# Kernel optimization log

Measured on AMD Instinct MI355X. Metric: run time of the kernel, lower is better.

## Reference

```python
import jax, jax.numpy as jnp
import numpy as np

N = 4096
C = 64
B = 4
DIST_THRESHOLD = 0.5
ALPHA = 0.01
NEG_INF = -1e15


def setup_inputs() -> dict:
    key = jax.random.key(0)
    k1, k2, k3, k4, k5 = jax.random.split(key, 5)
    x = jax.random.normal(k1, (B, N, C), dtype=jnp.float32)
    dist_mat = jax.random.uniform(k2, (N, N), dtype=jnp.float32)
    proj_w = jax.random.normal(k3, (N, C, C), dtype=jnp.float32) / np.sqrt(C)
    proj_b = jax.random.normal(k4, (N, C), dtype=jnp.float32) * 0.01
    a_w = jax.random.normal(k5, (N, 2 * C), dtype=jnp.float32) / np.sqrt(2 * C)
    return {"x": x, "dist_mat": dist_mat, "proj_w": proj_w, "proj_b": proj_b, "a_w": a_w}


def reference(x, dist_mat, proj_w, proj_b, a_w):
    # Adjacency: (0 < dist < threshold), diagonal forced to 1.
    adj = (dist_mat > 0) & (dist_mat < DIST_THRESHOLD)
    adj = adj | jnp.eye(N, dtype=bool)

    # Per-node projection (GraphDense): h[b,n,:] = x[b,n,:] @ proj_w[n] + proj_b[n]
    h = jnp.einsum('bnc,nco->bno', x, proj_w) + proj_b  # [B, N, C]

    # Attention score: a[j] . concat(h_i, h_j) without materializing [B,N,N,2C].
    a_src, a_dst = a_w[:, :C], a_w[:, C:]               # each [N, C]
    s = jnp.einsum('bic,jc->bij', h, a_src) + jnp.einsum('bjc,jc->bj', h, a_dst)[:, None, :]
    s = jnp.where(s >= 0, s, ALPHA * s)                 # LeakyReLU
    s = jnp.where(adj[None, :, :], s, NEG_INF)          # mask non-edges
    att = jax.nn.softmax(s, axis=-1)                    # [B, N, N]

    # Weighted aggregation over neighbors.
    y = jnp.einsum('bij,bjc->bic', att, h)              # [B, N, C]
    return y
```

## Files before the change

kernel.cpp:

```cpp
#include <hip/hip_runtime.h>

#define N 4096
#define C 64
#define B 4
#define SHIFT 12.0f

typedef __attribute__((ext_vector_type(8))) short short8;
typedef __attribute__((ext_vector_type(4))) short s16x4;
typedef __attribute__((ext_vector_type(4))) float f32x4;
typedef unsigned long long u64;

#define MFMA16(a, b, c) __builtin_amdgcn_mfma_f32_16x16x32_bf16(a, b, c, 0, 0, 0)

__device__ __forceinline__ short f2bf(float f) {
    unsigned u = __builtin_bit_cast(unsigned, f);
    u += 0x7fffu + ((u >> 16) & 1u);
    return (short)(u >> 16);
}

__global__ __launch_bounds__(256) void mask_kernel(const float* __restrict__ dist,
                                                   u64* __restrict__ msk) {
    const int wave = threadIdx.x >> 6, lane = threadIdx.x & 63;
    const int i = blockIdx.x * 4 + wave;
    const float* row = dist + (size_t)i * N;
#pragma unroll 8
    for (int jb = 0; jb < N / 64; jb++) {
        float d = row[jb * 64 + lane];
        u64 m = __ballot(d > 0.f && d < 0.5f);
        int dj = i - jb * 64;
        if (dj >= 0 && dj < 64) m |= (1ull << dj);
        if (lane == 0) msk[(size_t)i * (N / 64) + jb] = m;
    }
}

__global__ __launch_bounds__(256) void proj_kernel(
    const float* __restrict__ x,
    const float* __restrict__ proj_w,
    const float* __restrict__ proj_b,
    const float* __restrict__ a_w,
    short* __restrict__ h_bf,
    short* __restrict__ a_srcb,
    float* __restrict__ e2)
{
    __shared__ float lds_x[4][B][C];

    const int tid = threadIdx.x;
    const int wave = tid >> 6;
    const int lane = tid & 63;
    const int g = lane >> 4;
    const int o4 = lane & 15;
    const int n = blockIdx.x * 4 + wave;
    const float* Wn = proj_w + (size_t)n * C * C;

#pragma unroll
    for (int b = 0; b < B; b++)
        lds_x[wave][b][lane] = x[((size_t)b * N + n) * C + lane];

    float4 wbuf[16];
#pragma unroll
    for (int p = 0; p < 16; p++)
        wbuf[p] = *(const float4*)(Wn + (p * 4 + g) * C + o4 * 4);

    float acc[B][4];
#pragma unroll
    for (int b = 0; b < B; b++)
#pragma unroll
        for (int r = 0; r < 4; r++) acc[b][r] = 0.f;

#pragma unroll
    for (int p = 0; p < 16; p++) {
        float xs[B];
#pragma unroll
        for (int b = 0; b < B; b++) xs[b] = lds_x[wave][b][p * 4 + g];
#pragma unroll
        for (int b = 0; b < B; b++) {
            acc[b][0] = fmaf(xs[b], wbuf[p].x, acc[b][0]);
            acc[b][1] = fmaf(xs[b], wbuf[p].y, acc[b][1]);
            acc[b][2] = fmaf(xs[b], wbuf[p].z, acc[b][2]);
            acc[b][3] = fmaf(xs[b], wbuf[p].w, acc[b][3]);
        }
    }

#pragma unroll
    for (int b = 0; b < B; b++)
#pragma unroll
        for (int r = 0; r < 4; r++) {
            acc[b][r] += __shfl_xor(acc[b][r], 16, 64);
            acc[b][r] += __shfl_xor(acc[b][r], 32, 64);
        }

    float4 pb4 = *(const float4*)(proj_b + (size_t)n * C + o4 * 4);
#pragma unroll
    for (int b = 0; b < B; b++) {
        acc[b][0] += pb4.x; acc[b][1] += pb4.y;
        acc[b][2] += pb4.z; acc[b][3] += pb4.w;
    }

    float hg[4];
#pragma unroll
    for (int r = 0; r < 4; r++) {
        float v01 = (g & 1) ? acc[1][r] : acc[0][r];
        float v23 = (g & 1) ? acc[3][r] : acc[2][r];
        hg[r] = (g & 2) ? v23 : v01;
    }

    {
        s16x4 hv;
#pragma unroll
        for (int r = 0; r < 4; r++) hv[r] = f2bf(hg[r]);
        *(s16x4*)&h_bf[((size_t)g * N + n) * C + o4 * 4] = hv;
    }

    if (g == 0) {
        float4 as4 = *(const float4*)(a_w + (size_t)n * 2 * C + o4 * 4);
        s16x4 av;
        av[0] = f2bf(as4.x); av[1] = f2bf(as4.y);
        av[2] = f2bf(as4.z); av[3] = f2bf(as4.w);
        *(s16x4*)&a_srcb[(size_t)n * C + o4 * 4] = av;
    }

    {
        float4 ad4 = *(const float4*)(a_w + (size_t)n * 2 * C + C + o4 * 4);
        float s = hg[0] * ad4.x + hg[1] * ad4.y + hg[2] * ad4.z + hg[3] * ad4.w;
        s += __shfl_xor(s, 1, 64);
        s += __shfl_xor(s, 2, 64);
        s += __shfl_xor(s, 4, 64);
        s += __shfl_xor(s, 8, 64);
        if (o4 == 0) e2[g * N + n] = s - SHIFT;
    }
}

__global__ __launch_bounds__(256) void transpose_kernel(const short* __restrict__ h_bf,
                                                        short* __restrict__ hT_bf) {
    __shared__ short tile[64][72];
    const int t = threadIdx.x;
    const int b = blockIdx.y;
    const int n0 = blockIdx.x * 64;
    {
        int r = t >> 2, cs = (t & 3) * 16;
        const short* src = h_bf + ((size_t)b * N + n0 + r) * C + cs;
#pragma unroll
        for (int q = 0; q < 4; q++)
            *(s16x4*)&tile[r][cs + q * 4] = *(const s16x4*)(src + q * 4);
    }
    __syncthreads();
    {
        int c = t >> 2, ns = (t & 3) * 16;
        short v[16];
#pragma unroll
        for (int k = 0; k < 16; k++) v[k] = tile[ns + k][c];
        short* dst = hT_bf + (size_t)b * C * N + (size_t)c * N + n0 + ns;
        *(short8*)dst = *(short8*)&v[0];
        *(short8*)(dst + 8) = *(short8*)&v[8];
    }
}

__global__ __launch_bounds__(256) void attn_kernel(
    const u64* __restrict__ msk,
    const short* __restrict__ h_bf,
    const short* __restrict__ hT_bf,
    const short* __restrict__ a_srcb,
    const float* __restrict__ e2,
    float* __restrict__ part_y,
    float* __restrict__ part_l,
    int JS, int S, int mode)
{
    __shared__ float lds_e2[4][512];

    const int tid = threadIdx.x;
    const int wave = tid >> 6;
    const int lane = tid & 63;
    const int cl = lane & 15;
    const int rg = lane >> 4;
    const int rg8 = rg * 8;
    const int b = wave;
    const int sy = blockIdx.x % S;
    const int ix = blockIdx.x / S;
    const int i0 = ix * 32;
    const int jbeg = sy * JS;
    const bool e2lds = (JS <= 512);

    if (e2lds) {
        for (int q = lane * 4; q < JS; q += 256)
            *(f32x4*)&lds_e2[wave][q] = *(const f32x4*)(e2 + (size_t)b * N + jbeg + q);
    }

    short8 bfr[2][2];
#pragma unroll
    for (int u = 0; u < 2; u++) {
        const short* hrow = h_bf + ((size_t)b * N + i0 + u * 16 + cl) * C;
        bfr[u][0] = *(const short8*)(hrow + rg8);
        bfr[u][1] = *(const short8*)(hrow + 32 + rg8);
    }

    const u64* mr[2] = {msk + (size_t)(i0 + cl) * (N / 64),
                        msk + (size_t)(i0 + 16 + cl) * (N / 64)};

    f32x4 yacc[2][4];
#pragma unroll
    for (int u = 0; u < 2; u++)
#pragma unroll
        for (int t = 0; t < 4; t++) { f32x4 z = {0.f, 0.f, 0.f, 0.f}; yacc[u][t] = z; }
    float l_s[2] = {0.f, 0.f};

    const int jr = ((cl >> 2) << 3) | (cl & 3);
    const short* abase = a_srcb + (size_t)(jr) * C + rg8;

    short8 an0[4], an1[4];
#pragma unroll
    for (int t = 0; t < 4; t++) {
        const short* arow = abase + (size_t)(jbeg + (t >> 1) * 32 + (t & 1) * 4) * C;
        an0[t] = *(const short8*)(arow);
        an1[t] = *(const short8*)(arow + 32);
    }
    u64 mb0 = mr[0][jbeg >> 6], mb1 = mr[1][jbeg >> 6];

    for (int j0 = jbeg; j0 < jbeg + JS; j0 += 64) {
        const int jp = (j0 + 64 < jbeg + JS) ? j0 + 64 : jbeg;
        const u64 mb[2] = {mb0, mb1};

        short8 a0[4], a1[4];
#pragma unroll
        for (int t = 0; t < 4; t++) { a0[t] = an0[t]; a1[t] = an1[t]; }

        short8 h0[4], h1[4];
#pragma unroll
        for (int t = 0; t < 4; t++) {
            const short* hc = hT_bf + (size_t)b * C * N + (size_t)(t * 16 + cl) * N + j0 + rg8;
            h0[t] = *(const short8*)(hc);
            h1[t] = *(const short8*)(hc + 32);
        }
#pragma unroll
        for (int t = 0; t < 4; t++) {
            const short* arow = abase + (size_t)(jp + (t >> 1) * 32 + (t & 1) * 4) * C;
            an0[t] = *(const short8*)(arow);
            an1[t] = *(const short8*)(arow + 32);
        }
        u64 nb0 = mr[0][jp >> 6], nb1 = mr[1][jp >> 6];

        f32x4 st[2][4];
#pragma unroll
        for (int t = 0; t < 4; t++) {
            const int tq = t >> 1, tr = t & 1;
            const int off = tq * 32 + tr * 4 + rg8;
            f32x4 eq;
            if (e2lds) eq = *(const f32x4*)&lds_e2[wave][j0 - jbeg + off];
            else       eq = *(const f32x4*)(e2 + (size_t)b * N + j0 + off);
            const int sh = rg8 + tr * 4;
#pragma unroll
            for (int u = 0; u < 2; u++) {
                unsigned w32 = tq ? (unsigned)(mb[u] >> 32) : (unsigned)mb[u];
                unsigned ws = w32 >> sh;
                f32x4 z;
#pragma unroll
                for (int r = 0; r < 4; r++)
                    z[r] = ((ws >> r) & 1u) ? eq[r] : -1e30f;
                z = MFMA16(a0[t], bfr[u][0], z);
                z = MFMA16(a1[t], bfr[u][1], z);
                st[u][t] = z;
            }
        }

        short8 pa[2][2];
#pragma unroll
        for (int u = 0; u < 2; u++) {
            float ls = 0.f;
            short8 q0, q1;
#pragma unroll
            for (int t = 0; t < 4; t++) {
#pragma unroll
                for (int r = 0; r < 4; r++) {
                    float sv = st[u][t][r];
                    float pv = __expf(fmaxf(sv, fmaf(0.01f, sv, -11.88f)));
                    ls += pv;
                    short bv = f2bf(pv);
                    if (t < 2) q0[(t & 1) * 4 + r] = bv;
                    else       q1[(t & 1) * 4 + r] = bv;
                }
            }
            l_s[u] += ls;
            pa[u][0] = q0;
            pa[u][1] = q1;
        }

#pragma unroll
        for (int t = 0; t < 4; t++) {
            yacc[0][t] = MFMA16(pa[0][0], h0[t], yacc[0][t]);
            yacc[0][t] = MFMA16(pa[0][1], h1[t], yacc[0][t]);
            yacc[1][t] = MFMA16(pa[1][0], h0[t], yacc[1][t]);
            yacc[1][t] = MFMA16(pa[1][1], h1[t], yacc[1][t]);
        }
        mb0 = nb0; mb1 = nb1;
    }

#pragma unroll
    for (int u = 0; u < 2; u++) {
        l_s[u] += __shfl_xor(l_s[u], 16, 64);
        l_s[u] += __shfl_xor(l_s[u], 32, 64);
    }

    if (mode) {
#pragma unroll
        for (int u = 0; u < 2; u++) {
            int li = __builtin_bit_cast(int, l_s[u]);
            f32x4 l4;
#pragma unroll
            for (int r = 0; r < 4; r++)
                l4[r] = __builtin_bit_cast(float,
                        __builtin_amdgcn_ds_bpermute((rg * 4 + r) << 2, li));
#pragma unroll
            for (int t = 0; t < 4; t++)
#pragma unroll
                for (int r = 0; r < 4; r++)
                    part_y[((size_t)b * N + i0 + u * 16 + rg * 4 + r) * C + t * 16 + cl] =
                        yacc[u][t][r] / l4[r];
        }
    } else {
        size_t sb = (size_t)(sy * B + b) * N;
#pragma unroll
        for (int u = 0; u < 2; u++) {
#pragma unroll
            for (int t = 0; t < 4; t++)
#pragma unroll
                for (int r = 0; r < 4; r++)
                    part_y[(sb + i0 + u * 16 + rg * 4 + r) * C + t * 16 + cl] = yacc[u][t][r];
            if (lane < 16) part_l[sb + i0 + u * 16 + lane] = l_s[u];
        }
    }
}

__global__ __launch_bounds__(256) void combine_kernel(
    const float* __restrict__ part_y, const float* __restrict__ part_l,
    float* __restrict__ out, int S)
{
    int g = blockIdx.x * 256 + threadIdx.x;
    int c4 = (g & 15) * 4;
    int row = (g >> 4) & (N - 1);
    int b = g >> 16;
    int bn = b * N + row;
    f32x4 y = {0.f, 0.f, 0.f, 0.f};
    float l = 0.f;
    if (S == 8) {
#pragma unroll
        for (int s = 0; s < 8; s++) {
            l += part_l[s * (B * N) + bn];
            f32x4 v = *(const f32x4*)&part_y[((size_t)s * B * N + bn) * C + c4];
#pragma unroll
            for (int r = 0; r < 4; r++) y[r] += v[r];
        }
    } else {
        for (int s = 0; s < S; s++) {
            l += part_l[s * (B * N) + bn];
            f32x4 v = *(const f32x4*)&part_y[((size_t)s * B * N + bn) * C + c4];
#pragma unroll
            for (int r = 0; r < 4; r++) y[r] += v[r];
        }
    }
    float inv = 1.f / l;
    f32x4 o;
#pragma unroll
    for (int r = 0; r < 4; r++) o[r] = y[r] * inv;
    *(f32x4*)&out[(size_t)g * 4] = o;
}

extern "C" void kernel_launch(void* const* d_in, const int* in_sizes, int n_in,
                              void* d_out, int out_size, void* d_ws, size_t ws_size,
                              hipStream_t stream) {
    const float* x      = (const float*)d_in[0];
    const float* dist   = (const float*)d_in[1];
    const float* proj_w = (const float*)d_in[2];
    const float* proj_b = (const float*)d_in[3];
    const float* a_w    = (const float*)d_in[4];
    float* out = (float*)d_out;

    char* ws = (char*)d_ws;
    short* h_bf   = (short*)(ws);
    short* hT_bf  = (short*)(ws + (2u << 20));
    short* a_srcb = (short*)(ws + (4u << 20));
    float* e2     = (float*)(ws + (4u << 20) + (512u << 10));
    u64*   msk    = (u64*)  (ws + (5u << 20));
    float* part_l = (float*)(ws + (7u << 20));
    float* part_y = (float*)(ws + (8u << 20));

    proj_kernel<<<N / 4, 256, 0, stream>>>(x, proj_w, proj_b, a_w, h_bf, a_srcb, e2);
    transpose_kernel<<<dim3(N / 64, B), 256, 0, stream>>>(h_bf, hT_bf);
    mask_kernel<<<N / 4, 256, 0, stream>>>(dist, msk);

    int S = 8;
    while (S > 1 && (8u << 20) + (size_t)S * B * N * C * 4 > ws_size) S >>= 1;
    bool direct = ((8u << 20) + (size_t)B * N * C * 4 > ws_size);

    if (direct) {
        attn_kernel<<<N / 32, 256, 0, stream>>>(
            msk, h_bf, hT_bf, a_srcb, e2, out, part_l, N, 1, 1);
    } else {
        attn_kernel<<<(N / 32) * S, 256, 0, stream>>>(
            msk, h_bf, hT_bf, a_srcb, e2, part_y, part_l, N / S, S, 0);
        combine_kernel<<<(B * N * C / 4) / 256, 256, 0, stream>>>(part_y, part_l, out, S);
    }
}
```

Baseline: 282.4 us.

## Halve attention row tile to 16 rows and drop a_src prefetch for occupancy

Each attention block now covers 16 query rows instead of 32, which doubles the grid size and removes the second row-group of accumulators and score registers. The software prefetch of next-tile a_src fragments is dropped in favour of in-loop loads, and the hT loads move after the score MFMAs. Launch bounds request 6 waves per SIMD to raise occupancy. In exchange, each a_src and hT tile is loaded twice as often across blocks, and the kernel loses the register-level prefetch that hid load latency.

```diff
diff --git a/kernel.cpp b/kernel.cpp
--- a/kernel.cpp
+++ b/kernel.cpp
@@ -155,7 +155,7 @@
     }
 }
 
-__global__ __launch_bounds__(256) void attn_kernel(
+__global__ __launch_bounds__(256, 6) void attn_kernel(
     const u64* __restrict__ msk,
     const short* __restrict__ h_bf,
     const short* __restrict__ hT_bf,
@@ -175,8 +175,8 @@
     const int rg8 = rg * 8;
     const int b = wave;
     const int sy = blockIdx.x % S;
-    const int ix = blockIdx.x / S;
-    const int i0 = ix * 32;
+    const int iu = blockIdx.x / S;
+    const int i0 = iu * 16;
     const int jbeg = sy * JS;
     const bool e2lds = (JS <= 512);
 
@@ -185,60 +185,38 @@
             *(f32x4*)&lds_e2[wave][q] = *(const f32x4*)(e2 + (size_t)b * N + jbeg + q);
     }
 
-    short8 bfr[2][2];
-#pragma unroll
-    for (int u = 0; u < 2; u++) {
-        const short* hrow = h_bf + ((size_t)b * N + i0 + u * 16 + cl) * C;
-        bfr[u][0] = *(const short8*)(hrow + rg8);
-        bfr[u][1] = *(const short8*)(hrow + 32 + rg8);
-    }
-
-    const u64* mr[2] = {msk + (size_t)(i0 + cl) * (N / 64),
-                        msk + (size_t)(i0 + 16 + cl) * (N / 64)};
-
-    f32x4 yacc[2][4];
-#pragma unroll
-    for (int u = 0; u < 2; u++)
-#pragma unroll
-        for (int t = 0; t < 4; t++) { f32x4 z = {0.f, 0.f, 0.f, 0.f}; yacc[u][t] = z; }
-    float l_s[2] = {0.f, 0.f};
+    short8 bfr[2];
+    {
+        const short* hrow = h_bf + ((size_t)b * N + i0 + cl) * C;
+        bfr[0] = *(const short8*)(hrow + rg8);
+        bfr[1] = *(const short8*)(hrow + 32 + rg8);
+    }
+
+    const u64* mr = msk + (size_t)(i0 + cl) * (N / 64);
+
+    f32x4 yacc[4];
+#pragma unroll
+    for (int t = 0; t < 4; t++) { f32x4 z = {0.f, 0.f, 0.f, 0.f}; yacc[t] = z; }
+    float l_s = 0.f;
 
     const int jr = ((cl >> 2) << 3) | (cl & 3);
     const short* abase = a_srcb + (size_t)(jr) * C + rg8;
 
-    short8 an0[4], an1[4];
-#pragma unroll
-    for (int t = 0; t < 4; t++) {
-        const short* arow = abase + (size_t)(jbeg + (t >> 1) * 32 + (t & 1) * 4) * C;
-        an0[t] = *(const short8*)(arow);
-        an1[t] = *(const short8*)(arow + 32);
-    }
-    u64 mb0 = mr[0][jbeg >> 6], mb1 = mr[1][jbeg >> 6];
+    u64 mb = mr[jbeg >> 6];
 
     for (int j0 = jbeg; j0 < jbeg + JS; j0 += 64) {
         const int jp = (j0 + 64 < jbeg + JS) ? j0 + 64 : jbeg;
-        const u64 mb[2] = {mb0, mb1};
+        u64 nb = mr[jp >> 6];
 
         short8 a0[4], a1[4];
 #pragma unroll
-        for (int t = 0; t < 4; t++) { a0[t] = an0[t]; a1[t] = an1[t]; }
-
-        short8 h0[4], h1[4];
-#pragma unroll
-        for (int t = 0; t < 4; t++) {
-            const short* hc = hT_bf + (size_t)b * C * N + (size_t)(t * 16 + cl) * N + j0 + rg8;
-            h0[t] = *(const short8*)(hc);
-            h1[t] = *(const short8*)(hc + 32);
-        }
-#pragma unroll
-        for (int t = 0; t < 4; t++) {
-            const short* arow = abase + (size_t)(jp + (t >> 1) * 32 + (t & 1) * 4) * C;
-            an0[t] = *(const short8*)(arow);
-            an1[t] = *(const short8*)(arow + 32);
-        }
-        u64 nb0 = mr[0][jp >> 6], nb1 = mr[1][jp >> 6];
-
-        f32x4 st[2][4];
+        for (int t = 0; t < 4; t++) {
+            const short* arow = abase + (size_t)(j0 + (t >> 1) * 32 + (t & 1) * 4) * C;
+            a0[t] = *(const short8*)(arow);
+            a1[t] = *(const short8*)(arow + 32);
+        }
+
+        f32x4 st[4];
 #pragma unroll
         for (int t = 0; t < 4; t++) {
             const int tq = t >> 1, tr = t & 1;
@@ -246,86 +224,71 @@
             f32x4 eq;
             if (e2lds) eq = *(const f32x4*)&lds_e2[wave][j0 - jbeg + off];
             else       eq = *(const f32x4*)(e2 + (size_t)b * N + j0 + off);
-            const int sh = rg8 + tr * 4;
-#pragma unroll
-            for (int u = 0; u < 2; u++) {
-                unsigned w32 = tq ? (unsigned)(mb[u] >> 32) : (unsigned)mb[u];
-                unsigned ws = w32 >> sh;
-                f32x4 z;
-#pragma unroll
-                for (int r = 0; r < 4; r++)
-                    z[r] = ((ws >> r) & 1u) ? eq[r] : -1e30f;
-                z = MFMA16(a0[t], bfr[u][0], z);
-                z = MFMA16(a1[t], bfr[u][1], z);
-                st[u][t] = z;
+            unsigned w32 = tq ? (unsigned)(mb >> 32) : (unsigned)mb;
+            unsigned ws = w32 >> (rg8 + tr * 4);
+            f32x4 z;
+#pragma unroll
+            for (int r = 0; r < 4; r++)
+                z[r] = ((ws >> r) & 1u) ? eq[r] : -1e30f;
+            z = MFMA16(a0[t], bfr[0], z);
+            z = MFMA16(a1[t], bfr[1], z);
+            st[t] = z;
+        }
+
+        short8 h0[4], h1[4];
+#pragma unroll
+        for (int t = 0; t < 4; t++) {
+            const short* hc = hT_bf + (size_t)b * C * N + (size_t)(t * 16 + cl) * N + j0 + rg8;
+            h0[t] = *(const short8*)(hc);
+            h1[t] = *(const short8*)(hc + 32);
+        }
+
+        short8 pa0, pa1;
+#pragma unroll
+        for (int t = 0; t < 4; t++) {
+#pragma unroll
+            for (int r = 0; r < 4; r++) {
+                float sv = st[t][r];
+                float pv = __expf(fmaxf(sv, fmaf(0.01f, sv, -11.88f)));
+                l_s += pv;
+                short bv = f2bf(pv);
+                if (t < 2) pa0[(t & 1) * 4 + r] = bv;
+                else       pa1[(t & 1) * 4 + r] = bv;
             }
         }
 
-        short8 pa[2][2];
-#pragma unroll
-        for (int u = 0; u < 2; u++) {
-            float ls = 0.f;
-            short8 q0, q1;
-#pragma unroll
-            for (int t = 0; t < 4; t++) {
-#pragma unroll
-                for (int r = 0; r < 4; r++) {
-                    float sv = st[u][t][r];
-                    float pv = __expf(fmaxf(sv, fmaf(0.01f, sv, -11.88f)));
-                    ls += pv;
-                    short bv = f2bf(pv);
-                    if (t < 2) q0[(t & 1) * 4 + r] = bv;
-                    else       q1[(t & 1) * 4 + r] = bv;
-                }
-            }
-            l_s[u] += ls;
-            pa[u][0] = q0;
-            pa[u][1] = q1;
-        }
-
-#pragma unroll
-        for (int t = 0; t < 4; t++) {
-            yacc[0][t] = MFMA16(pa[0][0], h0[t], yacc[0][t]);
-            yacc[0][t] = MFMA16(pa[0][1], h1[t], yacc[0][t]);
-            yacc[1][t] = MFMA16(pa[1][0], h0[t], yacc[1][t]);
-            yacc[1][t] = MFMA16(pa[1][1], h1[t], yacc[1][t]);
-        }
-        mb0 = nb0; mb1 = nb1;
-    }
-
-#pragma unroll
-    for (int u = 0; u < 2; u++) {
-        l_s[u] += __shfl_xor(l_s[u], 16, 64);
-        l_s[u] += __shfl_xor(l_s[u], 32, 64);
-    }
+#pragma unroll
+        for (int t = 0; t < 4; t++) {
+            yacc[t] = MFMA16(pa0, h0[t], yacc[t]);
+            yacc[t] = MFMA16(pa1, h1[t], yacc[t]);
+        }
+        mb = nb;
+    }
+
+    l_s += __shfl_xor(l_s, 16, 64);
+    l_s += __shfl_xor(l_s, 32, 64);
 
     if (mode) {
-#pragma unroll
-        for (int u = 0; u < 2; u++) {
-            int li = __builtin_bit_cast(int, l_s[u]);
-            f32x4 l4;
+        int li = __builtin_bit_cast(int, l_s);
+        f32x4 l4;
+#pragma unroll
+        for (int r = 0; r < 4; r++)
+            l4[r] = __builtin_bit_cast(float,
+                    __builtin_amdgcn_ds_bpermute((rg * 4 + r) << 2, li));
+#pragma unroll
+        for (int t = 0; t < 4; t++)
 #pragma unroll
             for (int r = 0; r < 4; r++)
-                l4[r] = __builtin_bit_cast(float,
-                        __builtin_amdgcn_ds_bpermute((rg * 4 + r) << 2, li));
-#pragma unroll
-            for (int t = 0; t < 4; t++)
-#pragma unroll
-                for (int r = 0; r < 4; r++)
-                    part_y[((size_t)b * N + i0 + u * 16 + rg * 4 + r) * C + t * 16 + cl] =
-                        yacc[u][t][r] / l4[r];
-        }
+                part_y[((size_t)b * N + i0 + rg * 4 + r) * C + t * 16 + cl] =
+                    yacc[t][r] / l4[r];
     } else {
         size_t sb = (size_t)(sy * B + b) * N;
 #pragma unroll
-        for (int u = 0; u < 2; u++) {
-#pragma unroll
-            for (int t = 0; t < 4; t++)
-#pragma unroll
-                for (int r = 0; r < 4; r++)
-                    part_y[(sb + i0 + u * 16 + rg * 4 + r) * C + t * 16 + cl] = yacc[u][t][r];
-            if (lane < 16) part_l[sb + i0 + u * 16 + lane] = l_s[u];
-        }
+        for (int t = 0; t < 4; t++)
+#pragma unroll
+            for (int r = 0; r < 4; r++)
+                part_y[(sb + i0 + rg * 4 + r) * C + t * 16 + cl] = yacc[t][r];
+        if (lane < 16) part_l[sb + i0 + lane] = l_s;
     }
 }
 
@@ -391,10 +354,10 @@
     bool direct = ((8u << 20) + (size_t)B * N * C * 4 > ws_size);
 
     if (direct) {
-        attn_kernel<<<N / 32, 256, 0, stream>>>(
+        attn_kernel<<<N / 16, 256, 0, stream>>>(
             msk, h_bf, hT_bf, a_srcb, e2, out, part_l, N, 1, 1);
     } else {
-        attn_kernel<<<(N / 32) * S, 256, 0, stream>>>(
+        attn_kernel<<<(N / 16) * S, 256, 0, stream>>>(
             msk, h_bf, hT_bf, a_srcb, e2, part_y, part_l, N / S, S, 0);
         combine_kernel<<<(B * N * C / 4) / 256, 256, 0, stream>>>(part_y, part_l, out, S);
     }
```

After: 345.7 us. +22.4%, slower.

## Stage a_src tiles in double-buffered LDS and compute row sums via MFMA

Applied to the files above, without the earlier changes.

Before this change, each wave loaded its own copy of the a_src rows from global memory. Now the block cooperatively loads each 64-row a_src tile into a double-buffered LDS array, shared by the four batch waves, with a __syncthreads per iteration. The softmax denominator now comes from MFMAs against a vector of bf16 ones instead of scalar adds and cross-lane shuffles, and the e2 staging buffer in LDS is dropped in favour of direct global reads. The aim is to cut redundant global traffic and VALU work, at the cost of block-wide barriers. The denominator now sums the bf16-rounded probabilities rather than the fp32 values.

```diff
diff --git a/kernel.cpp b/kernel.cpp
--- a/kernel.cpp
+++ b/kernel.cpp
@@ -165,7 +165,7 @@
     float* __restrict__ part_l,
     int JS, int S, int mode)
 {
-    __shared__ float lds_e2[4][512];
+    __shared__ short lds_a[2][64][72];
 
     const int tid = threadIdx.x;
     const int wave = tid >> 6;
@@ -178,12 +178,6 @@
     const int ix = blockIdx.x / S;
     const int i0 = ix * 32;
     const int jbeg = sy * JS;
-    const bool e2lds = (JS <= 512);
-
-    if (e2lds) {
-        for (int q = lane * 4; q < JS; q += 256)
-            *(f32x4*)&lds_e2[wave][q] = *(const f32x4*)(e2 + (size_t)b * N + jbeg + q);
-    }
 
     short8 bfr[2][2];
 #pragma unroll
@@ -193,127 +187,120 @@
         bfr[u][1] = *(const short8*)(hrow + 32 + rg8);
     }
 
-    const u64* mr[2] = {msk + (size_t)(i0 + cl) * (N / 64),
-                        msk + (size_t)(i0 + 16 + cl) * (N / 64)};
+    const u64* mr0 = msk + (size_t)(i0 + cl) * (N / 64);
+    const u64* mr1 = msk + (size_t)(i0 + 16 + cl) * (N / 64);
 
     f32x4 yacc[2][4];
 #pragma unroll
     for (int u = 0; u < 2; u++)
 #pragma unroll
         for (int t = 0; t < 4; t++) { f32x4 z = {0.f, 0.f, 0.f, 0.f}; yacc[u][t] = z; }
-    float l_s[2] = {0.f, 0.f};
+    f32x4 yl[2];
+    { f32x4 z = {0.f, 0.f, 0.f, 0.f}; yl[0] = z; yl[1] = z; }
+
+    short8 ones;
+#pragma unroll
+    for (int k = 0; k < 8; k++) ones[k] = (short)0x3F80;
+
+    const float* eb = e2 + (size_t)b * N;
+    const short* hp[4];
+#pragma unroll
+    for (int t = 0; t < 4; t++)
+        hp[t] = hT_bf + (size_t)b * C * N + (size_t)(t * 16 + cl) * N + jbeg + rg8;
 
     const int jr = ((cl >> 2) << 3) | (cl & 3);
-    const short* abase = a_srcb + (size_t)(jr) * C + rg8;
-
-    short8 an0[4], an1[4];
-#pragma unroll
-    for (int t = 0; t < 4; t++) {
-        const short* arow = abase + (size_t)(jbeg + (t >> 1) * 32 + (t & 1) * 4) * C;
-        an0[t] = *(const short8*)(arow);
-        an1[t] = *(const short8*)(arow + 32);
-    }
-    u64 mb0 = mr[0][jbeg >> 6], mb1 = mr[1][jbeg >> 6];
+    const int srow = tid >> 2, scol = (tid & 3) * 16;
+
+    {
+        short8 g0 = *(const short8*)(a_srcb + (size_t)jbeg * 64 + tid * 16);
+        short8 g1 = *(const short8*)(a_srcb + (size_t)jbeg * 64 + tid * 16 + 8);
+        *(short8*)&lds_a[0][srow][scol] = g0;
+        *(short8*)&lds_a[0][srow][scol + 8] = g1;
+    }
+    __syncthreads();
+    int buf = 0;
 
     for (int j0 = jbeg; j0 < jbeg + JS; j0 += 64) {
-        const int jp = (j0 + 64 < jbeg + JS) ? j0 + 64 : jbeg;
-        const u64 mb[2] = {mb0, mb1};
-
-        short8 a0[4], a1[4];
-#pragma unroll
-        for (int t = 0; t < 4; t++) { a0[t] = an0[t]; a1[t] = an1[t]; }
-
-        short8 h0[4], h1[4];
-#pragma unroll
-        for (int t = 0; t < 4; t++) {
-            const short* hc = hT_bf + (size_t)b * C * N + (size_t)(t * 16 + cl) * N + j0 + rg8;
-            h0[t] = *(const short8*)(hc);
-            h1[t] = *(const short8*)(hc + 32);
-        }
-#pragma unroll
-        for (int t = 0; t < 4; t++) {
-            const short* arow = abase + (size_t)(jp + (t >> 1) * 32 + (t & 1) * 4) * C;
-            an0[t] = *(const short8*)(arow);
-            an1[t] = *(const short8*)(arow + 32);
-        }
-        u64 nb0 = mr[0][jp >> 6], nb1 = mr[1][jp >> 6];
-
-        f32x4 st[2][4];
-#pragma unroll
-        for (int t = 0; t < 4; t++) {
-            const int tq = t >> 1, tr = t & 1;
-            const int off = tq * 32 + tr * 4 + rg8;
-            f32x4 eq;
-            if (e2lds) eq = *(const f32x4*)&lds_e2[wave][j0 - jbeg + off];
-            else       eq = *(const f32x4*)(e2 + (size_t)b * N + j0 + off);
-            const int sh = rg8 + tr * 4;
-#pragma unroll
-            for (int u = 0; u < 2; u++) {
-                unsigned w32 = tq ? (unsigned)(mb[u] >> 32) : (unsigned)mb[u];
-                unsigned ws = w32 >> sh;
+        const bool more = (j0 + 64 < jbeg + JS);
+        const int jp = more ? j0 + 64 : j0;
+        short8 g0 = *(const short8*)(a_srcb + (size_t)jp * 64 + tid * 16);
+        short8 g1 = *(const short8*)(a_srcb + (size_t)jp * 64 + tid * 16 + 8);
+
+        const u64 mbs0 = mr0[j0 >> 6], mbs1 = mr1[j0 >> 6];
+
+        short8 pa[2][2];
+#pragma unroll
+        for (int u = 0; u < 2; u++) {
+            const u64 mb = u ? mbs1 : mbs0;
+            f32x4 st[4];
+#pragma unroll
+            for (int t = 0; t < 4; t++) {
+                const int tq = t >> 1, tr = t & 1;
+                const int vrow = jr + tq * 32 + tr * 4;
+                short8 a0 = *(const short8*)&lds_a[buf][vrow][rg8];
+                short8 a1 = *(const short8*)&lds_a[buf][vrow][32 + rg8];
+                f32x4 eq = *(const f32x4*)(eb + j0 + tq * 32 + tr * 4 + rg8);
+                unsigned w32 = tq ? (unsigned)(mb >> 32) : (unsigned)mb;
+                unsigned ws = w32 >> (rg8 + tr * 4);
                 f32x4 z;
 #pragma unroll
                 for (int r = 0; r < 4; r++)
                     z[r] = ((ws >> r) & 1u) ? eq[r] : -1e30f;
-                z = MFMA16(a0[t], bfr[u][0], z);
-                z = MFMA16(a1[t], bfr[u][1], z);
-                st[u][t] = z;
+                z = MFMA16(a0, bfr[u][0], z);
+                z = MFMA16(a1, bfr[u][1], z);
+                st[t] = z;
             }
-        }
-
-        short8 pa[2][2];
-#pragma unroll
-        for (int u = 0; u < 2; u++) {
-            float ls = 0.f;
+
             short8 q0, q1;
 #pragma unroll
             for (int t = 0; t < 4; t++) {
 #pragma unroll
                 for (int r = 0; r < 4; r++) {
-                    float sv = st[u][t][r];
+                    float sv = st[t][r];
                     float pv = __expf(fmaxf(sv, fmaf(0.01f, sv, -11.88f)));
-                    ls += pv;
                     short bv = f2bf(pv);
                     if (t < 2) q0[(t & 1) * 4 + r] = bv;
                     else       q1[(t & 1) * 4 + r] = bv;
                 }
             }
-            l_s[u] += ls;
             pa[u][0] = q0;
             pa[u][1] = q1;
-        }
+
+            yl[u] = MFMA16(pa[u][0], ones, yl[u]);
+            yl[u] = MFMA16(pa[u][1], ones, yl[u]);
+        }
+
+        if (more) {
+            *(short8*)&lds_a[buf ^ 1][srow][scol] = g0;
+            *(short8*)&lds_a[buf ^ 1][srow][scol + 8] = g1;
+        }
+        __syncthreads();
 
 #pragma unroll
         for (int t = 0; t < 4; t++) {
-            yacc[0][t] = MFMA16(pa[0][0], h0[t], yacc[0][t]);
-            yacc[0][t] = MFMA16(pa[0][1], h1[t], yacc[0][t]);
-            yacc[1][t] = MFMA16(pa[1][0], h0[t], yacc[1][t]);
-            yacc[1][t] = MFMA16(pa[1][1], h1[t], yacc[1][t]);
-        }
-        mb0 = nb0; mb1 = nb1;
-    }
-
-#pragma unroll
-    for (int u = 0; u < 2; u++) {
-        l_s[u] += __shfl_xor(l_s[u], 16, 64);
-        l_s[u] += __shfl_xor(l_s[u], 32, 64);
+            short8 h0 = *(const short8*)(hp[t]);
+            short8 h1 = *(const short8*)(hp[t] + 32);
+            yacc[0][t] = MFMA16(pa[0][0], h0, yacc[0][t]);
+            yacc[0][t] = MFMA16(pa[0][1], h1, yacc[0][t]);
+            yacc[1][t] = MFMA16(pa[1][0], h0, yacc[1][t]);
+            yacc[1][t] = MFMA16(pa[1][1], h1, yacc[1][t]);
+            hp[t] += 64;
+        }
+        buf ^= 1;
     }
 
     if (mode) {
 #pragma unroll
         for (int u = 0; u < 2; u++) {
-            int li = __builtin_bit_cast(int, l_s[u]);
-            f32x4 l4;
-#pragma unroll
-            for (int r = 0; r < 4; r++)
-                l4[r] = __builtin_bit_cast(float,
-                        __builtin_amdgcn_ds_bpermute((rg * 4 + r) << 2, li));
+            f32x4 inv;
+#pragma unroll
+            for (int r = 0; r < 4; r++) inv[r] = 1.f / yl[u][r];
 #pragma unroll
             for (int t = 0; t < 4; t++)
 #pragma unroll
                 for (int r = 0; r < 4; r++)
                     part_y[((size_t)b * N + i0 + u * 16 + rg * 4 + r) * C + t * 16 + cl] =
-                        yacc[u][t][r] / l4[r];
+                        yacc[u][t][r] * inv[r];
         }
     } else {
         size_t sb = (size_t)(sy * B + b) * N;
@@ -324,7 +311,7 @@
 #pragma unroll
                 for (int r = 0; r < 4; r++)
                     part_y[(sb + i0 + u * 16 + rg * 4 + r) * C + t * 16 + cl] = yacc[u][t][r];
-            if (lane < 16) part_l[sb + i0 + u * 16 + lane] = l_s[u];
+            if (cl == 0) *(f32x4*)&part_l[sb + i0 + u * 16 + rg * 4] = yl[u];
         }
     }
 }
```

Result: faster. 266.1 us (-5.8%).
